# Kernel tuning notes

Measured on AMD Instinct MI355X. Metric: run time of the kernel, lower is better.

Reference implementation:

```python
import jax, jax.numpy as jnp
import numpy as np

B, S, D = 4, 4096, 1024          # batch, seq, in/out features
H = 128                          # controller_hidden_dim
K = 8                            # num_spectral_bases
R = 8                            # low_rank_rank
OR = 8                           # orthogonal_rank
RES_SCALE = 1.0; SPEC_SCALE = 1.0; LR_SCALE = 1.0; ROT_SCALE = 1.0
LN_EPS = 1e-5


def setup_inputs() -> dict:
    key = jax.random.key(0)
    ks = jax.random.split(key, 16)
    g = lambda k, shape, scale=0.02: jax.random.normal(k, shape, jnp.float32) * scale
    return dict(
        x=jax.random.normal(ks[0], (B, S, D), jnp.float32),
        # base linear (teacher-aligned base)
        W_base=g(ks[1], (D, D)), b_base=jnp.zeros((D,), jnp.float32),
        # pooled-token conditioner: LayerNorm -> Linear -> GELU -> Linear
        ln_g=jnp.ones((D,), jnp.float32), ln_b=jnp.zeros((D,), jnp.float32),
        Wc1=g(ks[2], (D, H)), bc1=jnp.zeros((H,), jnp.float32),
        Wc2=g(ks[3], (H, H)), bc2=jnp.zeros((H,), jnp.float32),
        # gate heads
        W_rot_gate=g(ks[4], (H, 1)), b_rot_gate=jnp.zeros((1,), jnp.float32),
        W_rot_coeff=g(ks[5], (H, OR)), b_rot_coeff=jnp.zeros((OR,), jnp.float32),
        W_spec_gate=g(ks[6], (H, K)), b_spec_gate=jnp.zeros((K,), jnp.float32),
        W_lr_coeff=g(ks[7], (H, R)), b_lr_coeff=jnp.zeros((R,), jnp.float32),
        # spectral basis operator: input basis U, output basis V
        U_spec=g(ks[8], (K, D), 0.05), V_spec=g(ks[9], (K, D), 0.05),
        # low-rank residual operator
        U_lr=g(ks[10], (R, D), 0.05), V_lr=g(ks[11], (R, D), 0.05),
        # low-rank orthogonal mixer generators (skew-symmetric pairs)
        A_orth=g(ks[12], (OR, D), 0.05), B_orth=g(ks[13], (OR, D), 0.05),
    )


def reference(x, W_base, b_base, ln_g, ln_b, Wc1, bc1, Wc2, bc2,
              W_rot_gate, b_rot_gate, W_rot_coeff, b_rot_coeff,
              W_spec_gate, b_spec_gate, W_lr_coeff, b_lr_coeff,
              U_spec, V_spec, U_lr, V_lr, A_orth, B_orth):
    # --- pooled token conditioner: mean pool -> LN -> MLP -> hidden h [B,H]
    pooled = x.mean(axis=1)                                   # [B, D]
    mu = pooled.mean(-1, keepdims=True)
    var = pooled.var(-1, keepdims=True)
    z = (pooled - mu) * jax.lax.rsqrt(var + LN_EPS) * ln_g + ln_b
    h = jax.nn.gelu(z @ Wc1 + bc1) @ Wc2 + bc2                # [B, H]

    # --- conditioner-produced gates
    rot_gate = jax.nn.sigmoid(h @ W_rot_gate + b_rot_gate)    # [B, 1]
    rot_coeff = jnp.tanh(h @ W_rot_coeff + b_rot_coeff)       # [B, OR]
    spec_gate = jnp.tanh(h @ W_spec_gate + b_spec_gate)       # [B, K]
    lr_coeff = jnp.tanh(h @ W_lr_coeff + b_lr_coeff)          # [B, R]

    # --- low-rank orthogonal mixer: x_rot = x + gate * x @ G^T,
    #     G = sum_k c_k (a_k b_k^T - b_k a_k^T) (skew-symmetric generator)
    pa = jnp.einsum('bsi,ki->bsk', x, A_orth)
    pb = jnp.einsum('bsi,ki->bsk', x, B_orth)
    rot = (jnp.einsum('bsk,bk,ki->bsi', pb, rot_coeff, A_orth)
           - jnp.einsum('bsk,bk,ki->bsi', pa, rot_coeff, B_orth))
    x_rot = x + (ROT_SCALE * rot_gate)[:, None, :] * rot      # [B,S,D]

    # --- spectral basis operator: gated rank-K map through fixed bases
    s = jnp.einsum('bsi,ki->bsk', x_rot, U_spec)
    y_spec = SPEC_SCALE * jnp.einsum('bsk,bk,ko->bso', s, spec_gate, V_spec)

    # --- low-rank residual operator
    t = jnp.einsum('bsi,ki->bsk', x_rot, U_lr)
    y_lr = LR_SCALE * jnp.einsum('bsk,bk,ko->bso', t, lr_coeff, V_lr)

    # --- teacher-aligned base + gated residual operators
    return x_rot @ W_base + b_base + RES_SCALE * (y_spec + y_lr)
```

## Files before the change

kernel.cpp:

```cpp
#include <hip/hip_runtime.h>

typedef unsigned short u16;
typedef unsigned int   u32;
typedef __bf16 bf16x8 __attribute__((ext_vector_type(8)));
typedef float  f32x4  __attribute__((ext_vector_type(4)));

#define DD 1024

__device__ __forceinline__ u16 f2bf(float f) {
  u32 u = __float_as_uint(f);
  u32 r = (u + 0x7FFFu + ((u >> 16) & 1u)) >> 16;
  return (u16)r;
}

typedef const __attribute__((address_space(1))) void* gp1;
typedef __attribute__((address_space(3))) void* lp3;
__device__ __forceinline__ void gll16(const void* g, void* l) {
  __builtin_amdgcn_global_load_lds((gp1)g, (lp3)l, 16, 0, 0);
}

template <bool XB>
__global__ __launch_bounds__(256) void k01m(
    const float* __restrict__ x, u16* __restrict__ xb, float* __restrict__ pooled,
    const float* __restrict__ W,
    const float* __restrict__ Ao, const float* __restrict__ Bo,
    const float* __restrict__ Us, const float* __restrict__ Ul,
    float* __restrict__ AWBW, float* __restrict__ Mbuf,
    u16* __restrict__ Pb, u16* __restrict__ Wt,
    const float* __restrict__ lng, const float* __restrict__ lnb,
    const float* __restrict__ Wc1, float* __restrict__ h1pre,
    const float* Vs, const float* Vl,
    const float* bc1, const float* Wc2, const float* bc2,
    const float* Wrg, const float* brg, const float* Wrc, const float* brc,
    const float* Wsg, const float* bsg, const float* Wlc, const float* blc,
    float* __restrict__ gates, u16* __restrict__ RwT,
    u32* __restrict__ cntS, u32* __restrict__ cntH, u32* __restrict__ cntW) {
  __shared__ __align__(16) char shb[16384];
  const int tid = threadIdx.x;
  const int bid = blockIdx.x;

  if (bid >= 328 && bid < 840) {
    const int i = bid - 328;
    const int xcd = i & 7, local = i >> 3;
    const int rb = xcd * 64 + local;
    const int b = rb >> 7;
    const long r0 = (long)rb * 32;
    const char* xfb = (const char*)x;
    const int trow = tid >> 7;
    const int tcol = (tid & 127) * 8;
    float p[8];
#pragma unroll
    for (int j = 0; j < 8; j++) p[j] = 0.f;
    gll16(xfb + r0 * 4096 + tid * 16,        shb + tid * 16);
    gll16(xfb + (r0 + 1) * 4096 + tid * 16,  shb + 4096 + tid * 16);
    __syncthreads();
    int cur = 0;
    for (int c = 0; c < 16; c++) {
      if (c < 15) {
        const long rowb = (r0 + (long)(c + 1) * 2) * 4096;
        const int s = cur ^ 1;
        gll16(xfb + rowb + tid * 16,        shb + s * 8192 + tid * 16);
        gll16(xfb + rowb + 4096 + tid * 16, shb + s * 8192 + 4096 + tid * 16);
      }
      const char* bp = shb + cur * 8192 + trow * 4096 + (tid & 127) * 32;
      f32x4 u = *(const f32x4*)bp;
      f32x4 v = *(const f32x4*)(bp + 16);
      if (XB) {
        uint4 o;
        o.x = (u32)f2bf(u[0]) | ((u32)f2bf(u[1]) << 16);
        o.y = (u32)f2bf(u[2]) | ((u32)f2bf(u[3]) << 16);
        o.z = (u32)f2bf(v[0]) | ((u32)f2bf(v[1]) << 16);
        o.w = (u32)f2bf(v[2]) | ((u32)f2bf(v[3]) << 16);
        *(uint4*)((char*)xb + (r0 + (long)c * 2 + trow) * 2048 + (tid & 127) * 16) = o;
      }
      p[0] += u[0]; p[1] += u[1]; p[2] += u[2]; p[3] += u[3];
      p[4] += v[0]; p[5] += v[1]; p[6] += v[2]; p[7] += v[3];
      __syncthreads();
      cur ^= 1;
    }
    float* rsh = (float*)shb;
#pragma unroll
    for (int j = 0; j < 8; j++) rsh[tid * 8 + j] = p[j];
    __syncthreads();
    if (tid < 128) {
#pragma unroll
      for (int j = 0; j < 8; j++) {
        float sres = rsh[tid * 8 + j] + rsh[(tid + 128) * 8 + j];
        atomicAdd(&pooled[b * DD + tcol + j], sres);
      }
    }
    __syncthreads();
    if (tid == 0) atomicAdd(cntS, 1u);
    return;
  }
  if (bid < 64) {
    float (*red2)[128][16] = (float (*)[128][16])shb;
    const int m = bid;
    const int n = (m & 7) * 128 + (tid & 127), q = m >> 3, ih = tid >> 7;
    float acc[16];
#pragma unroll
    for (int k = 0; k < 16; k++) acc[k] = 0.f;
    const int ib = q * 128 + ih * 64;
    for (int i = ib; i < ib + 64; i++) {
      float wv = W[(long)i * DD + n];
#pragma unroll
      for (int k = 0; k < 8; k++) {
        acc[k]     += Ao[k * DD + i] * wv;
        acc[k + 8] += Bo[k * DD + i] * wv;
      }
    }
#pragma unroll
    for (int k = 0; k < 16; k++) red2[ih][tid & 127][k] = acc[k];
    __syncthreads();
    if (ih == 0)
#pragma unroll
      for (int k = 0; k < 16; k++)
        atomicAdd(&AWBW[k * DD + n], red2[0][tid][k] + red2[1][tid][k]);
    __syncthreads();
    if (tid == 0) atomicAdd(cntW, 1u);
  } else if (bid < 68) {
    float (*red)[4] = (float (*)[4])shb;
    const int m = bid - 64;
    const float* L  = (m == 0 || m == 2) ? Ao : Bo;
    const float* Rr = (m < 2) ? Us : Ul;
    const int o = tid >> 2, ch = tid & 3;
    const int k = o >> 3, kp = o & 7;
    float a = 0.f;
    for (int i = ch * 256; i < ch * 256 + 256; i++)
      a += L[(long)k * DD + i] * Rr[(long)kp * DD + i];
    red[o][ch] = a;
    __syncthreads();
    if (tid < 64) Mbuf[m * 64 + tid] = red[tid][0] + red[tid][1] + red[tid][2] + red[tid][3];
  } else if (bid < 72) {
    const int m = bid - 68;
    const float* src = m == 0 ? Ao : m == 1 ? Bo : m == 2 ? Us : Ul;
#pragma unroll
    for (int j = 0; j < 8; j++)
      for (int q = 0; q < 4; q++) {
        int i = q * 256 + tid;
        Pb[(m * 8 + j) * DD + i] = f2bf(src[j * DD + i]);
      }
  } else if (bid < 328) {
    u16 (*T)[66] = (u16 (*)[66])shb;
    const int t = bid - 72, tr = t >> 4, tc = t & 15;
#pragma unroll
    for (int q2 = 0; q2 < 16; q2++) {
      int idx = q2 * 256 + tid, r = idx >> 6, c = idx & 63;
      T[r][c] = f2bf(W[(long)(tr * 64 + r) * DD + tc * 64 + c]);
    }
    __syncthreads();
#pragma unroll
    for (int q2 = 0; q2 < 16; q2++) {
      int idx = q2 * 256 + tid, c = idx >> 6, r = idx & 63;
      Wt[(long)(tc * 64 + c) * DD + tr * 64 + r] = T[r][c];
    }
  } else if (bid < 872) {
    float* zs  = (float*)shb;
    float* red = (float*)(shb + 4096);
    const int lb = bid - 840;
    const int b = lb >> 3, ch = lb & 7;
    if (tid == 0) {
      while (atomicAdd(cntS, 0u) < 512u) __builtin_amdgcn_s_sleep(8);
    }
    __syncthreads();
    float4 v;
    v.x = atomicAdd(&pooled[b * DD + tid * 4 + 0], 0.f);
    v.y = atomicAdd(&pooled[b * DD + tid * 4 + 1], 0.f);
    v.z = atomicAdd(&pooled[b * DD + tid * 4 + 2], 0.f);
    v.w = atomicAdd(&pooled[b * DD + tid * 4 + 3], 0.f);
    v.x *= (1.f / 4096.f); v.y *= (1.f / 4096.f); v.z *= (1.f / 4096.f); v.w *= (1.f / 4096.f);
    float s = v.x + v.y + v.z + v.w;
    float sq = v.x * v.x + v.y * v.y + v.z * v.z + v.w * v.w;
    red[tid] = s; __syncthreads();
    for (int st = 128; st > 0; st >>= 1) { if (tid < st) red[tid] += red[tid + st]; __syncthreads(); }
    float mu = red[0] * (1.f / 1024.f);
    __syncthreads();
    red[tid] = sq; __syncthreads();
    for (int st = 128; st > 0; st >>= 1) { if (tid < st) red[tid] += red[tid + st]; __syncthreads(); }
    float var = red[0] * (1.f / 1024.f) - mu * mu;
    float rs = rsqrtf(var + 1e-5f);
    __syncthreads();
    {
      float4 g = *(const float4*)(lng + tid * 4);
      float4 be = *(const float4*)(lnb + tid * 4);
      zs[tid * 4 + 0] = (v.x - mu) * rs * g.x + be.x;
      zs[tid * 4 + 1] = (v.y - mu) * rs * g.y + be.y;
      zs[tid * 4 + 2] = (v.z - mu) * rs * g.z + be.z;
      zs[tid * 4 + 3] = (v.w - mu) * rs * g.w + be.w;
    }
    __syncthreads();
    const int j = tid & 127, half = tid >> 7;
    float a = 0.f;
#pragma unroll 8
    for (int dd = 0; dd < 64; dd++) {
      int ldi = half * 64 + dd;
      a += zs[ch * 128 + ldi] * Wc1[(long)ch * 16384 + ldi * 128 + j];
    }
    red[tid] = a;
    __syncthreads();
    if (tid < 128) atomicAdd(&h1pre[b * 128 + tid], red[tid] + red[tid + 128]);
    __syncthreads();
    if (tid == 0) atomicAdd(cntH, 1u);
  } else if (bid < 876) {
    float* h1s = (float*)shb;
    float* hb  = (float*)(shb + 512);
    float* red = (float*)(shb + 1024);
    float* hw  = (float*)(shb + 2048);
    const int b = bid - 872;
    for (int idx = tid; idx < 3200; idx += 256) {
      float vv;
      if (idx < 128)       vv = Wrg[idx];
      else if (idx < 1152) vv = Wrc[idx - 128];
      else if (idx < 2176) vv = Wsg[idx - 1152];
      else                 vv = Wlc[idx - 2176];
      hw[idx] = vv;
    }
    if (tid == 0) {
      while (atomicAdd(cntH, 0u) < 32u) __builtin_amdgcn_s_sleep(8);
    }
    __syncthreads();
    if (tid < 128) {
      float hv = atomicAdd(&h1pre[b * 128 + tid], 0.f) + bc1[tid];
      float th = tanhf(0.7978845608028654f * (hv + 0.044715f * hv * hv * hv));
      h1s[tid] = 0.5f * hv * (1.f + th);
    }
    __syncthreads();
    const int i = tid & 127, half = tid >> 7;
    float a = 0.f;
#pragma unroll 8
    for (int k = 0; k < 64; k++) {
      int kk = half * 64 + k;
      a += h1s[kk] * Wc2[kk * 128 + i];
    }
    red[tid] = a;
    __syncthreads();
    if (tid < 128) hb[tid] = red[tid] + red[tid + 128] + bc2[tid];
    __syncthreads();
    if (tid < 25) {
      float acc;
      if (tid == 0) {
        acc = brg[0];
        for (int k = 0; k < 128; k++) acc += hb[k] * hw[k];
        red[0] = 1.f / (1.f + expf(-acc));
      } else if (tid < 9) {
        int ci = tid - 1; acc = brc[ci];
        for (int k = 0; k < 128; k++) acc += hb[k] * hw[128 + k * 8 + ci];
        red[tid] = tanhf(acc);
      } else if (tid < 17) {
        int ci = tid - 9; acc = bsg[ci];
        for (int k = 0; k < 128; k++) acc += hb[k] * hw[1152 + k * 8 + ci];
        red[tid] = tanhf(acc);
      } else {
        int ci = tid - 17; acc = blc[ci];
        for (int k = 0; k < 128; k++) acc += hb[k] * hw[2176 + k * 8 + ci];
        red[tid] = tanhf(acc);
      }
    }
    __syncthreads();
    if (tid < 24) {
      float g = red[0];
      gates[b * 32 + tid] = (tid < 8) ? g * red[1 + tid] : red[1 + tid];
    }
  } else {
    if (tid == 0) {
      while (atomicAdd(cntW, 0u) < 64u) __builtin_amdgcn_s_sleep(8);
    }
    __syncthreads();
    const int n = (int)(bid - 876) * 256 + tid;
#pragma unroll
    for (int j = 0; j < 8; j++) {
      RwT[n * 32 + j]      = f2bf(atomicAdd(&AWBW[j * DD + n], 0.f));
      RwT[n * 32 + 8 + j]  = f2bf(atomicAdd(&AWBW[(8 + j) * DD + n], 0.f));
      RwT[n * 32 + 16 + j] = f2bf(Vs[(long)j * DD + n]);
      RwT[n * 32 + 24 + j] = f2bf(Vl[(long)j * DD + n]);
    }
  }
}

__global__ __launch_bounds__(256, 2) void k3b_fused(
    const u16* __restrict__ xb, const u16* __restrict__ Wt,
    const u16* __restrict__ Pb, const float* __restrict__ gates,
    const float* __restrict__ Mbuf, const u16* __restrict__ RwT,
    const float* __restrict__ bb, float* __restrict__ out) {
  __shared__ __align__(16) char smem[54400];
  const int tid = threadIdx.x, lane = tid & 63, w = tid >> 6;
  const int quad = lane >> 4, lrow = lane & 15;
  const int g = blockIdx.x;
  const int xcd = g & 7, local = g >> 3;
  const int bm = xcd * 16 + (local >> 2);
  const int bn2 = local & 3;
  const long m0 = (long)bm * 128;
  const int n0 = bn2 * 256;
  const int batch = bm >> 5;
  float* Ml = (float*)(smem + 53248);
  float* gl = (float*)(smem + 54272);
  Ml[tid] = Mbuf[tid];
  if (tid < 24) gl[tid] = gates[batch * 32 + tid];
  const int mw = (w & 1) * 64, nw = (w >> 1) * 128;
  const int pc0 = (w >> 1) * 16;
  const int sr = lane >> 2, sc = (lane & 3) * 16;
  const char* xbp = (const char*)xb;
  const char* wtp = (const char*)Wt;
  const char* pbp = (const char*)Pb;
  const long aOff0 = (m0 + (long)w * 16 + sr) * 2048 + sc;
  const long aOff1 = aOff0 + 64 * 2048;
  const long bOff  = ((long)n0 + w * 16 + sr) * 2048 + sc;
  const long pOff  = ((long)w * 16 + sr) * 2048 + sc;
  const int d0 = w * 1024 + lane * 16;

  f32x4 acc[4][8] = {};
  f32x4 acc2[4] = {};

  gll16(xbp + aOff0, smem + d0);
  gll16(xbp + aOff1, smem + d0 + 4096);
#pragma unroll
  for (int seg = 0; seg < 4; seg++)
    gll16(wtp + bOff + (long)seg * 64 * 2048, smem + 16384 + seg * 4096 + d0);
  if (w < 2) gll16(pbp + pOff, smem + 49152 + d0);
  __syncthreads();

  int cur = 0;
  for (int kc = 0; kc < 32; kc++) {
    if (kc < 31) {
      const long ko = (long)(kc + 1) * 64;
      const int s = cur ^ 1;
      gll16(xbp + aOff0 + ko, smem + s * 8192 + d0);
      gll16(xbp + aOff1 + ko, smem + s * 8192 + d0 + 4096);
#pragma unroll
      for (int seg = 0; seg < 4; seg++)
        gll16(wtp + bOff + (long)seg * 64 * 2048 + ko,
              smem + 16384 + s * 16384 + seg * 4096 + d0);
      if (w < 2) gll16(pbp + pOff + ko, smem + 49152 + s * 2048 + d0);
    }
    const u16* At = (const u16*)(smem + cur * 8192);
    const u16* Bt = (const u16*)(smem + 16384 + cur * 16384);
    const u16* Pt = (const u16*)(smem + 49152 + cur * 2048);
    bf16x8 af[4], bq[8], bp;
#pragma unroll
    for (int tm = 0; tm < 4; tm++)
      af[tm] = *(const bf16x8*)(At + (mw + tm * 16 + lrow) * 32 + quad * 8);
#pragma unroll
    for (int tn = 0; tn < 8; tn++)
      bq[tn] = *(const bf16x8*)(Bt + (nw + tn * 16 + lrow) * 32 + quad * 8);
    bp = *(const bf16x8*)(Pt + (pc0 + lrow) * 32 + quad * 8);
#pragma unroll
    for (int tm = 0; tm < 4; tm++)
#pragma unroll
      for (int tn = 0; tn < 8; tn++)
        acc[tm][tn] = __builtin_amdgcn_mfma_f32_16x16x32_bf16(af[tm], bq[tn], acc[tm][tn], 0, 0, 0);
#pragma unroll
    for (int tm = 0; tm < 4; tm++)
      acc2[tm] = __builtin_amdgcn_mfma_f32_16x16x32_bf16(af[tm], bp, acc2[tm], 0, 0, 0);
    __syncthreads();
    cur ^= 1;
  }

  {
    const long rOff = ((long)n0 + w * 16 + sr) * 64 + sc;
#pragma unroll
    for (int seg = 0; seg < 4; seg++)
      gll16((const char*)RwT + rOff + (long)seg * 64 * 64,
            smem + 16384 + seg * 4096 + d0);
  }
  float* projF = (float*)smem;
#pragma unroll
  for (int tm = 0; tm < 4; tm++)
#pragma unroll
    for (int r = 0; r < 4; r++) {
      int row = mw + tm * 16 + quad * 4 + r;
      int col = pc0 + lrow;
      projF[row * 32 + (col ^ (row & 31))] = acc2[tm][r];
    }
  __syncthreads();
  if (tid < 128) {
    float pr[32];
#pragma unroll
    for (int j = 0; j < 32; j++) pr[j] = projF[tid * 32 + (j ^ (tid & 31))];
    float wo[32];
#pragma unroll
    for (int k = 0; k < 8; k++) { wo[k] = gl[k] * pr[8 + k]; wo[8 + k] = -gl[k] * pr[k]; }
#pragma unroll
    for (int kp = 0; kp < 8; kp++) {
      float sv = pr[16 + kp], tv = pr[24 + kp];
#pragma unroll
      for (int k = 0; k < 8; k++) {
        float gpb = gl[k] * pr[8 + k], gpa = gl[k] * pr[k];
        sv += gpb * Ml[k * 8 + kp]       - gpa * Ml[64 + k * 8 + kp];
        tv += gpb * Ml[128 + k * 8 + kp] - gpa * Ml[192 + k * 8 + kp];
      }
      wo[16 + kp] = gl[8 + kp] * sv;
      wo[24 + kp] = gl[16 + kp] * tv;
    }
    u16* wLds = (u16*)(smem + 32768);
#pragma unroll
    for (int j = 0; j < 32; j++) wLds[tid * 32 + j] = f2bf(wo[j]);
  }
  __syncthreads();
  {
    const u16* wL = (const u16*)(smem + 32768);
    const u16* Rt = (const u16*)(smem + 16384);
    bf16x8 af[4], bq[8];
#pragma unroll
    for (int tm = 0; tm < 4; tm++)
      af[tm] = *(const bf16x8*)(wL + (mw + tm * 16 + lrow) * 32 + quad * 8);
#pragma unroll
    for (int tn = 0; tn < 8; tn++)
      bq[tn] = *(const bf16x8*)(Rt + (nw + tn * 16 + lrow) * 32 + quad * 8);
#pragma unroll
    for (int tm = 0; tm < 4; tm++)
#pragma unroll
      for (int tn = 0; tn < 8; tn++)
        acc[tm][tn] = __builtin_amdgcn_mfma_f32_16x16x32_bf16(af[tm], bq[tn], acc[tm][tn], 0, 0, 0);
  }
#pragma unroll
  for (int tn = 0; tn < 8; tn++) {
    const int col = n0 + nw + tn * 16 + lrow;
    const float bias = bb[col];
#pragma unroll
    for (int tm = 0; tm < 4; tm++)
#pragma unroll
      for (int r = 0; r < 4; r++) {
        long row = m0 + mw + tm * 16 + quad * 4 + r;
        out[row * DD + col] = acc[tm][tn][r] + bias;
      }
  }
}

template <bool XB>
__global__ __launch_bounds__(256) void k3_fused(
    const float* __restrict__ xf, const u16* __restrict__ xb,
    const u16* __restrict__ Wt, const u16* __restrict__ Pb,
    const float* __restrict__ gates, const float* __restrict__ Mbuf,
    const u16* __restrict__ RwT, const float* __restrict__ bb,
    float* __restrict__ out) {
  __shared__ __align__(16) u16 At[4096];
  __shared__ __align__(16) u16 Bt[4096];
  __shared__ __align__(16) u16 Pt[1024];
  __shared__ float projF[128 * 32];
  __shared__ __align__(16) u16 wLds[4096];
  __shared__ float Ml[256];
  __shared__ float gl[24];
  const int tid = threadIdx.x, lane = tid & 63, w = tid >> 6;
  const int quad = lane >> 4, lrow = lane & 15;
  const int bn = blockIdx.x & 7, bm = blockIdx.x >> 3;
  const long m0 = (long)bm * 128;
  const int n0 = bn * 128;
  const int batch = bm >> 5;
  Ml[tid] = Mbuf[tid];
  if (tid < 24) gl[tid] = gates[batch * 32 + tid];
  const int mw = (w & 1) * 64, nw = (w >> 1) * 64;
  const int p0 = (w * 2) * 1024 + lane * 16, p1 = p0 + 1024;
  f32x4 acc[4][4] = {};
  f32x4 acc2[2][2] = {};
  for (int kc = 0; kc < 32; kc++) {
    uint4 vb0 = *(const uint4*)((const char*)Wt + (long)(n0 + (p0 >> 6)) * 2048 + kc * 64 + (p0 & 63));
    uint4 vb1 = *(const uint4*)((const char*)Wt + (long)(n0 + (p1 >> 6)) * 2048 + kc * 64 + (p1 & 63));
    uint4 vp;
    if (tid < 128)
      vp = *(const uint4*)((const char*)Pb + (tid >> 2) * 2048 + kc * 64 + (tid & 3) * 16);
    if (XB) {
      uint4 va0 = *(const uint4*)((const char*)xb + (m0 + (p0 >> 6)) * 2048 + kc * 64 + (p0 & 63));
      uint4 va1 = *(const uint4*)((const char*)xb + (m0 + (p1 >> 6)) * 2048 + kc * 64 + (p1 & 63));
      *(uint4*)((char*)At + p0) = va0;
      *(uint4*)((char*)At + p1) = va1;
    } else {
      ushort4 oa[4];
#pragma unroll
      for (int i = 0; i < 4; i++) {
        int fi = i * 256 + tid, row = fi >> 3, c4 = (fi & 7) * 4;
        float4 v = *(const float4*)(xf + (m0 + row) * DD + kc * 32 + c4);
        oa[i].x = f2bf(v.x); oa[i].y = f2bf(v.y); oa[i].z = f2bf(v.z); oa[i].w = f2bf(v.w);
      }
#pragma unroll
      for (int i = 0; i < 4; i++) {
        int fi = i * 256 + tid, row = fi >> 3, c4 = (fi & 7) * 4;
        *(ushort4*)(At + row * 32 + c4) = oa[i];
      }
    }
    *(uint4*)((char*)Bt + p0) = vb0;
    *(uint4*)((char*)Bt + p1) = vb1;
    if (tid < 128) *(uint4*)((char*)Pt + (tid >> 2) * 64 + (tid & 3) * 16) = vp;
    __syncthreads();
    bf16x8 af[4], bq[4], af2[2], bp[2];
#pragma unroll
    for (int tm = 0; tm < 4; tm++)
      af[tm] = *(const bf16x8*)(At + (mw + tm * 16 + lrow) * 32 + quad * 8);
#pragma unroll
    for (int tn = 0; tn < 4; tn++)
      bq[tn] = *(const bf16x8*)(Bt + (nw + tn * 16 + lrow) * 32 + quad * 8);
#pragma unroll
    for (int t2 = 0; t2 < 2; t2++)
      af2[t2] = *(const bf16x8*)(At + (w * 32 + t2 * 16 + lrow) * 32 + quad * 8);
#pragma unroll
    for (int tn2 = 0; tn2 < 2; tn2++)
      bp[tn2] = *(const bf16x8*)(Pt + (tn2 * 16 + lrow) * 32 + quad * 8);
#pragma unroll
    for (int tm = 0; tm < 4; tm++)
#pragma unroll
      for (int tn = 0; tn < 4; tn++)
        acc[tm][tn] = __builtin_amdgcn_mfma_f32_16x16x32_bf16(af[tm], bq[tn], acc[tm][tn], 0, 0, 0);
#pragma unroll
    for (int t2 = 0; t2 < 2; t2++)
#pragma unroll
      for (int tn2 = 0; tn2 < 2; tn2++)
        acc2[t2][tn2] = __builtin_amdgcn_mfma_f32_16x16x32_bf16(af2[t2], bp[tn2], acc2[t2][tn2], 0, 0, 0);
    __syncthreads();
  }
#pragma unroll
  for (int t2 = 0; t2 < 2; t2++)
#pragma unroll
    for (int tn2 = 0; tn2 < 2; tn2++)
#pragma unroll
      for (int r = 0; r < 4; r++)
        projF[(w * 32 + t2 * 16 + quad * 4 + r) * 32 + tn2 * 16 + lrow] = acc2[t2][tn2][r];
  {
    uint4 vr0 = *(const uint4*)((const char*)RwT + (long)(n0 + (p0 >> 6)) * 64 + (p0 & 63));
    uint4 vr1 = *(const uint4*)((const char*)RwT + (long)(n0 + (p1 >> 6)) * 64 + (p1 & 63));
    *(uint4*)((char*)Bt + p0) = vr0;
    *(uint4*)((char*)Bt + p1) = vr1;
  }
  __syncthreads();
  if (tid < 128) {
    float pr[32];
#pragma unroll
    for (int j = 0; j < 32; j++) pr[j] = projF[tid * 32 + j];
    float wo[32];
#pragma unroll
    for (int k = 0; k < 8; k++) { wo[k] = gl[k] * pr[8 + k]; wo[8 + k] = -gl[k] * pr[k]; }
#pragma unroll
    for (int kp = 0; kp < 8; kp++) {
      float sv = pr[16 + kp], tv = pr[24 + kp];
#pragma unroll
      for (int k = 0; k < 8; k++) {
        float gpb = gl[k] * pr[8 + k], gpa = gl[k] * pr[k];
        sv += gpb * Ml[k * 8 + kp]       - gpa * Ml[64 + k * 8 + kp];
        tv += gpb * Ml[128 + k * 8 + kp] - gpa * Ml[192 + k * 8 + kp];
      }
      wo[16 + kp] = gl[8 + kp] * sv;
      wo[24 + kp] = gl[16 + kp] * tv;
    }
#pragma unroll
    for (int j = 0; j < 32; j++) wLds[tid * 32 + j] = f2bf(wo[j]);
  }
  __syncthreads();
  {
    bf16x8 af[4], bq[4];
#pragma unroll
    for (int tm = 0; tm < 4; tm++)
      af[tm] = *(const bf16x8*)(wLds + (mw + tm * 16 + lrow) * 32 + quad * 8);
#pragma unroll
    for (int tn = 0; tn < 4; tn++)
      bq[tn] = *(const bf16x8*)(Bt + (nw + tn * 16 + lrow) * 32 + quad * 8);
#pragma unroll
    for (int tm = 0; tm < 4; tm++)
#pragma unroll
      for (int tn = 0; tn < 4; tn++)
        acc[tm][tn] = __builtin_amdgcn_mfma_f32_16x16x32_bf16(af[tm], bq[tn], acc[tm][tn], 0, 0, 0);
  }
#pragma unroll
  for (int tn = 0; tn < 4; tn++) {
    const int col = n0 + nw + tn * 16 + lrow;
    const float bias = bb[col];
#pragma unroll
    for (int tm = 0; tm < 4; tm++)
#pragma unroll
      for (int r = 0; r < 4; r++) {
        long row = m0 + mw + tm * 16 + quad * 4 + r;
        out[row * DD + col] = acc[tm][tn][r] + bias;
      }
  }
}

extern "C" void kernel_launch(void* const* d_in, const int* in_sizes, int n_in,
                              void* d_out, int out_size, void* d_ws, size_t ws_size,
                              hipStream_t stream) {
  const float* x   = (const float*)d_in[0];
  const float* Wb  = (const float*)d_in[1];
  const float* bb  = (const float*)d_in[2];
  const float* lng = (const float*)d_in[3];
  const float* lnb = (const float*)d_in[4];
  const float* Wc1 = (const float*)d_in[5];
  const float* bc1 = (const float*)d_in[6];
  const float* Wc2 = (const float*)d_in[7];
  const float* bc2 = (const float*)d_in[8];
  const float* Wrg = (const float*)d_in[9];
  const float* brg = (const float*)d_in[10];
  const float* Wrc = (const float*)d_in[11];
  const float* brc = (const float*)d_in[12];
  const float* Wsg = (const float*)d_in[13];
  const float* bsg = (const float*)d_in[14];
  const float* Wlc = (const float*)d_in[15];
  const float* blc = (const float*)d_in[16];
  const float* Us  = (const float*)d_in[17];
  const float* Vs  = (const float*)d_in[18];
  const float* Ul  = (const float*)d_in[19];
  const float* Vl  = (const float*)d_in[20];
  const float* Ao  = (const float*)d_in[21];
  const float* Bo  = (const float*)d_in[22];

  char* ws = (char*)d_ws;
  float* pooled = (float*)(ws + 0);
  float* AWBW   = (float*)(ws + 16384);
  float* h1pre  = (float*)(ws + 81920);
  float* gates  = (float*)(ws + 83968);
  float* Mbuf   = (float*)(ws + 84480);
  u32*   cntH   = (u32*)  (ws + 85504);
  u32*   cntS   = (u32*)  (ws + 85508);
  u32*   cntW   = (u32*)  (ws + 85512);
  u16*   RwT    = (u16*)  (ws + 85568);
  u16*   Pb     = (u16*)  (ws + 151104);
  u16*   Wt     = (u16*)  (ws + 216640);
  u16*   xb     = (u16*)  (ws + 2313792);
  float* out    = (float*)d_out;

  const bool modeA = ws_size >= (size_t)2313792 + 33554432;

  (void)hipMemsetAsync(d_ws, 0, 85568, stream);
  if (modeA) {
    k01m<true><<<880, 256, 0, stream>>>(x, xb, pooled, Wb, Ao, Bo, Us, Ul,
                                        AWBW, Mbuf, Pb, Wt,
                                        lng, lnb, Wc1, h1pre, Vs, Vl,
                                        bc1, Wc2, bc2, Wrg, brg, Wrc, brc,
                                        Wsg, bsg, Wlc, blc, gates, RwT,
                                        cntS, cntH, cntW);
    k3b_fused<<<512, 256, 0, stream>>>(xb, Wt, Pb, gates, Mbuf, RwT, bb, out);
  } else {
    k01m<false><<<880, 256, 0, stream>>>(x, xb, pooled, Wb, Ao, Bo, Us, Ul,
                                         AWBW, Mbuf, Pb, Wt,
                                         lng, lnb, Wc1, h1pre, Vs, Vl,
                                         bc1, Wc2, bc2, Wrg, brg, Wrc, brc,
                                         Wsg, bsg, Wlc, blc, gates, RwT,
                                         cntS, cntH, cntW);
    k3_fused<false><<<1024, 256, 0, stream>>>(x, xb, Wt, Pb, gates, Mbuf, RwT, bb, out);
  }
}
```

Baseline: 264.2 us.

## Triple-buffer LDS pipelines with vmcnt-based waits in GEMM and pooling kernels

Both the fused bf16 GEMM main loop and the x pooling/conversion stage move from double to triple buffering. Prefetch now runs two stages ahead, and the full __syncthreads is replaced by explicit s_waitcnt vmcnt counts plus a raw s_barrier, so global-to-LDS loads overlap more compute. The GEMM kernel's LDS grows from about 54 KB to 81 KB per block, which may cut occupancy below the two blocks per CU named in launch_bounds. The hand-counted vmcnt values depend on the exact number of outstanding loads per wave, which is fragile.

Measured after the change: 264.6 us. No clear change (+0.2%).

```diff
diff --git a/kernel.cpp b/kernel.cpp
--- a/kernel.cpp
+++ b/kernel.cpp
@@ -18,6 +18,8 @@
 __device__ __forceinline__ void gll16(const void* g, void* l) {
   __builtin_amdgcn_global_load_lds((gp1)g, (lp3)l, 16, 0, 0);
 }
+
+#define SBAR0 __builtin_amdgcn_sched_barrier(0)
 
 template <bool XB>
 __global__ __launch_bounds__(256) void k01m(
@@ -35,7 +37,7 @@
     const float* Wsg, const float* bsg, const float* Wlc, const float* blc,
     float* __restrict__ gates, u16* __restrict__ RwT,
     u32* __restrict__ cntS, u32* __restrict__ cntH, u32* __restrict__ cntW) {
-  __shared__ __align__(16) char shb[16384];
+  __shared__ __align__(16) char shb[24576];
   const int tid = threadIdx.x;
   const int bid = blockIdx.x;
 
@@ -51,17 +53,18 @@
     float p[8];
 #pragma unroll
     for (int j = 0; j < 8; j++) p[j] = 0.f;
-    gll16(xfb + r0 * 4096 + tid * 16,        shb + tid * 16);
-    gll16(xfb + (r0 + 1) * 4096 + tid * 16,  shb + 4096 + tid * 16);
-    __syncthreads();
-    int cur = 0;
+    auto issueS = [&](int c, int bi) {
+      const long rowb = (r0 + (long)c * 2) * 4096;
+      gll16(xfb + rowb + tid * 16,        shb + bi * 8192 + tid * 16);
+      gll16(xfb + rowb + 4096 + tid * 16, shb + bi * 8192 + 4096 + tid * 16);
+    };
+    issueS(0, 0); issueS(1, 1);
+    asm volatile("s_waitcnt vmcnt(2)" ::: "memory");
+    SBAR0; __builtin_amdgcn_s_barrier(); SBAR0;
+#pragma unroll
     for (int c = 0; c < 16; c++) {
-      if (c < 15) {
-        const long rowb = (r0 + (long)(c + 1) * 2) * 4096;
-        const int s = cur ^ 1;
-        gll16(xfb + rowb + tid * 16,        shb + s * 8192 + tid * 16);
-        gll16(xfb + rowb + 4096 + tid * 16, shb + s * 8192 + 4096 + tid * 16);
-      }
+      const int cur = c % 3;
+      if (c + 2 < 16) issueS(c + 2, (c + 2) % 3);
       const char* bp = shb + cur * 8192 + trow * 4096 + (tid & 127) * 32;
       f32x4 u = *(const f32x4*)bp;
       f32x4 v = *(const f32x4*)(bp + 16);
@@ -75,9 +78,17 @@
       }
       p[0] += u[0]; p[1] += u[1]; p[2] += u[2]; p[3] += u[3];
       p[4] += v[0]; p[5] += v[1]; p[6] += v[2]; p[7] += v[3];
-      __syncthreads();
-      cur ^= 1;
-    }
+      if (c + 2 < 16) {
+        if (XB) asm volatile("s_waitcnt vmcnt(3)" ::: "memory");
+        else    asm volatile("s_waitcnt vmcnt(2)" ::: "memory");
+        SBAR0; __builtin_amdgcn_s_barrier(); SBAR0;
+      } else if (c == 14) {
+        if (XB) asm volatile("s_waitcnt vmcnt(2)" ::: "memory");
+        else    asm volatile("s_waitcnt vmcnt(0)" ::: "memory");
+        SBAR0; __builtin_amdgcn_s_barrier(); SBAR0;
+      }
+    }
+    __syncthreads();
     float* rsh = (float*)shb;
 #pragma unroll
     for (int j = 0; j < 8; j++) rsh[tid * 8 + j] = p[j];
@@ -282,7 +293,7 @@
     const u16* __restrict__ Pb, const float* __restrict__ gates,
     const float* __restrict__ Mbuf, const u16* __restrict__ RwT,
     const float* __restrict__ bb, float* __restrict__ out) {
-  __shared__ __align__(16) char smem[54400];
+  __shared__ __align__(16) char smem[81024];
   const int tid = threadIdx.x, lane = tid & 63, w = tid >> 6;
   const int quad = lane >> 4, lrow = lane & 15;
   const int g = blockIdx.x;
@@ -292,8 +303,8 @@
   const long m0 = (long)bm * 128;
   const int n0 = bn2 * 256;
   const int batch = bm >> 5;
-  float* Ml = (float*)(smem + 53248);
-  float* gl = (float*)(smem + 54272);
+  float* Ml = (float*)(smem + 79872);
+  float* gl = (float*)(smem + 80896);
   Ml[tid] = Mbuf[tid];
   if (tid < 24) gl[tid] = gates[batch * 32 + tid];
   const int mw = (w & 1) * 64, nw = (w >> 1) * 128;
@@ -311,30 +322,20 @@
   f32x4 acc[4][8] = {};
   f32x4 acc2[4] = {};
 
-  gll16(xbp + aOff0, smem + d0);
-  gll16(xbp + aOff1, smem + d0 + 4096);
-#pragma unroll
-  for (int seg = 0; seg < 4; seg++)
-    gll16(wtp + bOff + (long)seg * 64 * 2048, smem + 16384 + seg * 4096 + d0);
-  if (w < 2) gll16(pbp + pOff, smem + 49152 + d0);
-  __syncthreads();
-
-  int cur = 0;
-  for (int kc = 0; kc < 32; kc++) {
-    if (kc < 31) {
-      const long ko = (long)(kc + 1) * 64;
-      const int s = cur ^ 1;
-      gll16(xbp + aOff0 + ko, smem + s * 8192 + d0);
-      gll16(xbp + aOff1 + ko, smem + s * 8192 + d0 + 4096);
-#pragma unroll
-      for (int seg = 0; seg < 4; seg++)
-        gll16(wtp + bOff + (long)seg * 64 * 2048 + ko,
-              smem + 16384 + s * 16384 + seg * 4096 + d0);
-      if (w < 2) gll16(pbp + pOff + ko, smem + 49152 + s * 2048 + d0);
-    }
-    const u16* At = (const u16*)(smem + cur * 8192);
-    const u16* Bt = (const u16*)(smem + 16384 + cur * 16384);
-    const u16* Pt = (const u16*)(smem + 49152 + cur * 2048);
+  auto issue = [&](int kc, int bi) {
+    const long ko = (long)kc * 64;
+    gll16(xbp + aOff0 + ko, smem + bi * 8192 + d0);
+    gll16(xbp + aOff1 + ko, smem + bi * 8192 + d0 + 4096);
+#pragma unroll
+    for (int seg = 0; seg < 4; seg++)
+      gll16(wtp + bOff + (long)seg * 131072 + ko,
+            smem + 24576 + bi * 16384 + seg * 4096 + d0);
+    if (w < 2) gll16(pbp + pOff + ko, smem + 73728 + bi * 2048 + d0);
+  };
+  auto compute = [&](int bi) {
+    const u16* At = (const u16*)(smem + bi * 8192);
+    const u16* Bt = (const u16*)(smem + 24576 + bi * 16384);
+    const u16* Pt = (const u16*)(smem + 73728 + bi * 2048);
     bf16x8 af[4], bq[8], bp;
 #pragma unroll
     for (int tm = 0; tm < 4; tm++)
@@ -351,16 +352,36 @@
 #pragma unroll
     for (int tm = 0; tm < 4; tm++)
       acc2[tm] = __builtin_amdgcn_mfma_f32_16x16x32_bf16(af[tm], bp, acc2[tm], 0, 0, 0);
-    __syncthreads();
-    cur ^= 1;
-  }
+  };
+
+  issue(0, 0); issue(1, 1);
+  if (w < 2) asm volatile("s_waitcnt vmcnt(7)" ::: "memory");
+  else       asm volatile("s_waitcnt vmcnt(6)" ::: "memory");
+  SBAR0; __builtin_amdgcn_s_barrier(); SBAR0;
+
+  int cur = 0;
+  for (int kc = 0; kc < 30; kc++) {
+    int nb = cur - 1; if (nb < 0) nb = 2;
+    issue(kc + 2, nb);
+    compute(cur);
+    if (w < 2) asm volatile("s_waitcnt vmcnt(7)" ::: "memory");
+    else       asm volatile("s_waitcnt vmcnt(6)" ::: "memory");
+    SBAR0; __builtin_amdgcn_s_barrier(); SBAR0;
+    cur = (cur == 2) ? 0 : cur + 1;
+  }
+  compute(cur);
+  asm volatile("s_waitcnt vmcnt(0)" ::: "memory");
+  SBAR0; __builtin_amdgcn_s_barrier(); SBAR0;
+  cur = (cur == 2) ? 0 : cur + 1;
+  compute(cur);
+  __syncthreads();
 
   {
     const long rOff = ((long)n0 + w * 16 + sr) * 64 + sc;
 #pragma unroll
     for (int seg = 0; seg < 4; seg++)
-      gll16((const char*)RwT + rOff + (long)seg * 64 * 64,
-            smem + 16384 + seg * 4096 + d0);
+      gll16((const char*)RwT + rOff + (long)seg * 4096,
+            smem + 24576 + seg * 4096 + d0);
   }
   float* projF = (float*)smem;
 #pragma unroll
@@ -391,14 +412,14 @@
       wo[16 + kp] = gl[8 + kp] * sv;
       wo[24 + kp] = gl[16 + kp] * tv;
     }
-    u16* wLds = (u16*)(smem + 32768);
+    u16* wLds = (u16*)(smem + 40960);
 #pragma unroll
     for (int j = 0; j < 32; j++) wLds[tid * 32 + j] = f2bf(wo[j]);
   }
   __syncthreads();
   {
-    const u16* wL = (const u16*)(smem + 32768);
-    const u16* Rt = (const u16*)(smem + 16384);
+    const u16* wL = (const u16*)(smem + 40960);
+    const u16* Rt = (const u16*)(smem + 24576);
     bf16x8 af[4], bq[8];
 #pragma unroll
     for (int tm = 0; tm < 4; tm++)
```
